# Performance work log

Measured on AMD Instinct MI355X. Metric: run time of the kernel, lower is better.

## Reference

```python
import jax, jax.numpy as jnp
import numpy as np

D_MODEL = 1024
HIDDEN = 4096
N_EXPERTS = 8
TOP_K = 2
BATCH, SEQ = 4, 4096


def setup_inputs() -> dict:
    key = jax.random.key(0)
    k1, k2, k3, k4 = jax.random.split(key, 4)
    s_in = 1.0 / np.sqrt(D_MODEL)
    s_h = 1.0 / np.sqrt(HIDDEN)
    return {
        "x": jax.random.normal(k1, (BATCH, SEQ, D_MODEL), dtype=jnp.float32),
        "gate_w": jax.random.normal(k2, (D_MODEL, N_EXPERTS), dtype=jnp.float32) * s_in,
        "w1": jax.random.normal(k3, (N_EXPERTS, D_MODEL, HIDDEN), dtype=jnp.float32) * s_in,
        "w2": jax.random.normal(k4, (N_EXPERTS, HIDDEN, D_MODEL), dtype=jnp.float32) * s_h,
    }


def reference(x, gate_w, w1, w2):
    orig_shape = x.shape
    xf = x.reshape(-1, x.shape[-1])  # [T, d]
    scores = xf @ gate_w  # [T, E]
    expert_weights, expert_indices = jax.lax.top_k(scores, TOP_K)  # [T, K]
    expert_weights = jax.nn.softmax(expert_weights, axis=-1)  # softmax over top-k only

    output = jnp.zeros_like(xf)
    for i in range(N_EXPERTS):
        # per-token combine weight for expert i (0 if not routed to i)
        sel = (expert_indices == i)  # [T, K]
        wts = jnp.sum(jnp.where(sel, expert_weights, 0.0), axis=-1)  # [T]
        h = jax.nn.silu(xf @ w1[i])  # [T, H]
        expert_out = h @ w2[i]  # [T, d]
        output = output + wts[:, None] * expert_out
    return output.reshape(orig_shape)
```

## Files before the change

kernel.cpp:

```cpp
#include <hip/hip_runtime.h>
#include <cstdint>
#include <cstddef>

#define T_TOKENS 16384
#define DMODEL 1024
#define HID 4096
#define NEXP 8
#define NPAIRS 32768

typedef _Float16 half8 __attribute__((ext_vector_type(8)));
typedef _Float16 half4 __attribute__((ext_vector_type(4)));
typedef float f32x4 __attribute__((ext_vector_type(4)));

__device__ __forceinline__ void gload_lds16(const void* g, void* l) {
  __builtin_amdgcn_global_load_lds(
      (const __attribute__((address_space(1))) unsigned int*)g,
      (__attribute__((address_space(3))) unsigned int*)l, 16, 0, 0);
}

__global__ __launch_bounds__(256) void k_gate(const float* __restrict__ x,
                                              const float* __restrict__ gw,
                                              int2* __restrict__ route_e,
                                              float2* __restrict__ route_w,
                                              int* __restrict__ counts) {
  __shared__ int lcnt[NEXP];
  int tid = threadIdx.x, lane = tid & 63, w = tid >> 6;
  if (tid < NEXP) lcnt[tid] = 0;
  __syncthreads();
  int t = blockIdx.x * 4 + w;
  const float4* xr = (const float4*)(x + (size_t)t * DMODEL);
  double s[NEXP];
#pragma unroll
  for (int e = 0; e < NEXP; e++) s[e] = 0.0;
#pragma unroll
  for (int j = 0; j < 4; j++) {
    float4 v = xr[lane + 64 * j];
    int d0 = (lane + 64 * j) * 4;
    const float* vv = (const float*)&v;
#pragma unroll
    for (int q = 0; q < 4; q++) {
      float xv = vv[q];
      const float4* g = (const float4*)(gw + (size_t)(d0 + q) * NEXP);
      float4 g0 = g[0], g1 = g[1];
      s[0] += (double)xv * g0.x; s[1] += (double)xv * g0.y;
      s[2] += (double)xv * g0.z; s[3] += (double)xv * g0.w;
      s[4] += (double)xv * g1.x; s[5] += (double)xv * g1.y;
      s[6] += (double)xv * g1.z; s[7] += (double)xv * g1.w;
    }
  }
  for (int m = 1; m < 64; m <<= 1) {
#pragma unroll
    for (int e = 0; e < NEXP; e++) s[e] += __shfl_xor(s[e], m);
  }
  if (lane == 0) {
    double m0 = -1e300; int e0 = 0;
#pragma unroll
    for (int e = 0; e < NEXP; e++) if (s[e] > m0) { m0 = s[e]; e0 = e; }
    double m1 = -1e300; int e1 = (e0 == 0) ? 1 : 0;
#pragma unroll
    for (int e = 0; e < NEXP; e++) if (e != e0 && s[e] > m1) { m1 = s[e]; e1 = e; }
    double ew = exp(m1 - m0);
    float w0 = (float)(1.0 / (1.0 + ew));
    float w1v = (float)(ew / (1.0 + ew));
    route_e[t] = make_int2(e0, e1);
    route_w[t] = make_float2(w0, w1v);
    atomicAdd(&lcnt[e0], 1);
    atomicAdd(&lcnt[e1], 1);
  }
  __syncthreads();
  if (tid < NEXP && lcnt[tid]) atomicAdd(&counts[tid], lcnt[tid]);
}

__global__ void k_prefix(const int* __restrict__ counts, int* __restrict__ offsets,
                         int* __restrict__ cursors) {
  if (threadIdx.x == 0) {
    int a = 0;
    for (int e = 0; e < NEXP; e++) { offsets[e] = a; cursors[e] = a; a += counts[e]; }
  }
}

__global__ __launch_bounds__(256) void k_assign(const int2* __restrict__ route_e,
                                                const float2* __restrict__ route_w,
                                                int* __restrict__ cursors,
                                                int* __restrict__ tok,
                                                float* __restrict__ wtp) {
  __shared__ int lcnt[NEXP];
  __shared__ int lbase[NEXP];
  int tid = threadIdx.x;
  int t = blockIdx.x * 256 + tid;
  if (tid < NEXP) lcnt[tid] = 0;
  __syncthreads();
  int2 e = route_e[t];
  float2 w = route_w[t];
  int r0 = atomicAdd(&lcnt[e.x], 1);
  int r1 = atomicAdd(&lcnt[e.y], 1);
  __syncthreads();
  if (tid < NEXP) lbase[tid] = lcnt[tid] ? atomicAdd(&cursors[tid], lcnt[tid]) : 0;
  __syncthreads();
  int p0 = lbase[e.x] + r0; tok[p0] = t; wtp[p0] = w.x;
  int p1 = lbase[e.y] + r1; tok[p1] = t; wtp[p1] = w.y;
}

__global__ __launch_bounds__(256) void k_cvt_x(const float* __restrict__ x,
                                               _Float16* __restrict__ xh) {
  int i = blockIdx.x * 256 + threadIdx.x;
  float4 v = ((const float4*)x)[i];
  half4 o = { (_Float16)v.x, (_Float16)v.y, (_Float16)v.z, (_Float16)v.w };
  ((half4*)xh)[i] = o;
}

__global__ __launch_bounds__(256) void k_tcvt(const float* __restrict__ in,
                                              _Float16* __restrict__ out,
                                              int R, int C) {
  __shared__ _Float16 tile[64][72];
  int e = blockIdx.z, tc = blockIdx.x, tr = blockIdx.y;
  const float* src = in + ((size_t)e * R + (size_t)tr * 64) * C + (size_t)tc * 64;
  int rr = threadIdx.x >> 4, c4 = (threadIdx.x & 15) * 4;
#pragma unroll
  for (int it = 0; it < 4; it++) {
    int r = rr + it * 16;
    float4 v = *(const float4*)(src + (size_t)r * C + c4);
    tile[r][c4 + 0] = (_Float16)v.x; tile[r][c4 + 1] = (_Float16)v.y;
    tile[r][c4 + 2] = (_Float16)v.z; tile[r][c4 + 3] = (_Float16)v.w;
  }
  __syncthreads();
  _Float16* dst = out + ((size_t)e * C + (size_t)tc * 64) * R + (size_t)tr * 64;
#pragma unroll
  for (int it = 0; it < 4; it++) {
    int c = rr + it * 16;
    half4 o = { tile[c4 + 0][c], tile[c4 + 1][c], tile[c4 + 2][c], tile[c4 + 3][c] };
    *(half4*)(dst + (size_t)c * R + c4) = o;
  }
}

template <int MODE>
__global__ __launch_bounds__(256) void k_gemm(
    const _Float16* __restrict__ A, const _Float16* __restrict__ B,
    const int* __restrict__ counts, const int* __restrict__ offsets,
    const int* __restrict__ tok, const float* __restrict__ wtp,
    _Float16* __restrict__ Hout, float* __restrict__ out,
    int A_stride, int B_row_stride, int B_k_off, int K_len, int n0_global, int CH) {
  int e = blockIdx.x >> 7;
  int tm = blockIdx.x & 127;
  int n_e = counts[e];
  if (tm * 128 >= n_e) return;
  int seg = offsets[e];

  __shared__ _Float16 As[128 * 64];
  __shared__ _Float16 Bs[128 * 64];

  int tid = threadIdx.x, lane = tid & 63, wid = tid >> 6;
  int wr = wid >> 1, wc = wid & 1;
  int colbase = n0_global + blockIdx.y * 128;

  const _Float16* asrc[4];
  const _Float16* bsrc[4];
  const _Float16* Bexp = B + (size_t)e * ((size_t)DMODEL * HID);
#pragma unroll
  for (int c = 0; c < 4; c++) {
    int rloc = wid * 32 + c * 8 + (lane >> 3);
    int ridx = min(tm * 128 + rloc, n_e - 1);
    size_t arow;
    if (MODE == 0) arow = (size_t)tok[seg + ridx];
    else           arow = (size_t)(seg + ridx);
    asrc[c] = A + arow * (size_t)A_stride + ((lane & 7) * 8);
    int nloc = wid * 32 + c * 8 + (lane >> 3);
    bsrc[c] = Bexp + (size_t)(colbase + nloc) * B_row_stride + B_k_off + ((lane & 7) * 8);
  }

  f32x4 acc[4][4];
#pragma unroll
  for (int m = 0; m < 4; m++)
#pragma unroll
    for (int n = 0; n < 4; n++) acc[m][n] = (f32x4){0.f, 0.f, 0.f, 0.f};

  for (int k0 = 0; k0 < K_len; k0 += 64) {
#pragma unroll
    for (int c = 0; c < 4; c++) {
      gload_lds16(asrc[c] + k0, As + (wid * 4 + c) * 512);
      gload_lds16(bsrc[c] + k0, Bs + (wid * 4 + c) * 512);
    }
    __syncthreads();
#pragma unroll
    for (int kk = 0; kk < 64; kk += 32) {
      half8 af[4], bf[4];
#pragma unroll
      for (int m = 0; m < 4; m++)
        af[m] = *(const half8*)(As + (wr * 64 + m * 16 + (lane & 15)) * 64 + kk + ((lane >> 4) * 8));
#pragma unroll
      for (int n = 0; n < 4; n++)
        bf[n] = *(const half8*)(Bs + (wc * 64 + n * 16 + (lane & 15)) * 64 + kk + ((lane >> 4) * 8));
#pragma unroll
      for (int m = 0; m < 4; m++)
#pragma unroll
        for (int n = 0; n < 4; n++)
          acc[m][n] = __builtin_amdgcn_mfma_f32_16x16x32_f16(af[m], bf[n], acc[m][n], 0, 0, 0);
    }
    __syncthreads();
  }

  int cbase = wc * 64 + (lane & 15);
#pragma unroll
  for (int m = 0; m < 4; m++) {
    int rb = wr * 64 + m * 16 + ((lane >> 4) << 2);
#pragma unroll
    for (int r = 0; r < 4; r++) {
      int grow = tm * 128 + rb + r;
      if (grow >= n_e) continue;
      int gp = seg + grow;
      if (MODE == 0) {
        _Float16* hrow = Hout + (size_t)gp * CH + blockIdx.y * 128 + cbase;
#pragma unroll
        for (int n = 0; n < 4; n++) {
          float v = acc[m][n][r];
          float sv = v / (1.f + __expf(-v));
          hrow[n * 16] = (_Float16)sv;
        }
      } else {
        float wt = wtp[gp];
        int t = tok[gp];
        float* orow = out + (size_t)t * DMODEL + colbase + cbase;
#pragma unroll
        for (int n = 0; n < 4; n++)
          atomicAdd(orow + n * 16, wt * acc[m][n][r]);
      }
    }
  }
}

extern "C" void kernel_launch(void* const* d_in, const int* in_sizes, int n_in,
                              void* d_out, int out_size, void* d_ws, size_t ws_size,
                              hipStream_t stream) {
  const float* x  = (const float*)d_in[0];
  const float* gw = (const float*)d_in[1];
  const float* w1 = (const float*)d_in[2];
  const float* w2 = (const float*)d_in[3];
  float* out = (float*)d_out;

  char* p = (char*)d_ws;
  int* counts  = (int*)p;
  int* cursors = (int*)(p + 64);
  int* offsets = (int*)(p + 128);
  p += 4096;
  int2*   route_e = (int2*)p;   p += (size_t)T_TOKENS * 8;
  float2* route_w = (float2*)p; p += (size_t)T_TOKENS * 8;
  int*    tok = (int*)p;        p += (size_t)NPAIRS * 4;
  float*  wtp = (float*)p;      p += (size_t)NPAIRS * 4;
  _Float16* xh  = (_Float16*)p; p += (size_t)T_TOKENS * DMODEL * 2;
  _Float16* w1T = (_Float16*)p; p += (size_t)NEXP * DMODEL * HID * 2;
  _Float16* w2T = (_Float16*)p; p += (size_t)NEXP * DMODEL * HID * 2;
  size_t used = (size_t)(p - (char*)d_ws);
  int CH = HID;
  while (CH > 256 && used + (size_t)NPAIRS * CH * 2 > ws_size) CH >>= 1;
  _Float16* Hbuf = (_Float16*)p;

  hipMemsetAsync(counts, 0, 4096, stream);
  hipMemsetAsync(out, 0, (size_t)out_size * 4, stream);

  k_cvt_x<<<T_TOKENS * DMODEL / 4 / 256, 256, 0, stream>>>(x, xh);
  k_tcvt<<<dim3(HID / 64, DMODEL / 64, NEXP), 256, 0, stream>>>(w1, w1T, DMODEL, HID);
  k_tcvt<<<dim3(DMODEL / 64, HID / 64, NEXP), 256, 0, stream>>>(w2, w2T, HID, DMODEL);
  k_gate<<<T_TOKENS / 4, 256, 0, stream>>>(x, gw, route_e, route_w, counts);
  k_prefix<<<1, 64, 0, stream>>>(counts, offsets, cursors);
  k_assign<<<T_TOKENS / 256, 256, 0, stream>>>(route_e, route_w, cursors, tok, wtp);

  for (int h0 = 0; h0 < HID; h0 += CH) {
    k_gemm<0><<<dim3(NEXP * 128, CH / 128), 256, 0, stream>>>(
        xh, w1T, counts, offsets, tok, wtp, Hbuf, nullptr,
        DMODEL, DMODEL, 0, DMODEL, h0, CH);
    k_gemm<1><<<dim3(NEXP * 128, DMODEL / 128), 256, 0, stream>>>(
        Hbuf, w2T, counts, offsets, tok, wtp, nullptr, out,
        CH, HID, h0, CH, 0, CH);
  }
}
```

Measured before the change: 1.591 ms.

## Enlarge grouped GEMM tiles to 256x256 with triple-buffered async LDS pipeline

Reworks the expert GEMM kernel to use 512-thread blocks computing 256x256 output tiles, with each wave holding an 8x4 grid of MFMA accumulators. The K loop now runs in 32-wide steps through a three-stage LDS ring filled by global_load_lds, prefetching two steps ahead and using explicit vmcnt waits, barriers and setprio around the MFMA block. The goals are more data reuse per LDS load and overlap of global memory traffic with compute. The costs are higher register and LDS use (96 KB of LDS per block), fewer blocks in flight, and more wasted work on partly filled 256-row expert tiles.

```diff
diff --git a/kernel.cpp b/kernel.cpp
--- a/kernel.cpp
+++ b/kernel.cpp
@@ -134,95 +134,134 @@
 }
 
 template <int MODE>
-__global__ __launch_bounds__(256) void k_gemm(
+__global__ __launch_bounds__(512, 2) void k_gemm(
     const _Float16* __restrict__ A, const _Float16* __restrict__ B,
     const int* __restrict__ counts, const int* __restrict__ offsets,
     const int* __restrict__ tok, const float* __restrict__ wtp,
     _Float16* __restrict__ Hout, float* __restrict__ out,
-    int A_stride, int B_row_stride, int B_k_off, int K_len, int n0_global, int CH) {
+    int A_stride, int B_row_stride, int B_k_off, int NT, int n0_global, int CH) {
   int e = blockIdx.x >> 7;
   int tm = blockIdx.x & 127;
   int n_e = counts[e];
-  if (tm * 128 >= n_e) return;
+  if (tm * 256 >= n_e) return;
   int seg = offsets[e];
 
-  __shared__ _Float16 As[128 * 64];
-  __shared__ _Float16 Bs[128 * 64];
+  __shared__ _Float16 lds[49152];
 
   int tid = threadIdx.x, lane = tid & 63, wid = tid >> 6;
-  int wr = wid >> 1, wc = wid & 1;
-  int colbase = n0_global + blockIdx.y * 128;
-
-  const _Float16* asrc[4];
-  const _Float16* bsrc[4];
+  int wr = wid >> 2, wc = wid & 3;
+  int ri = lane & 15, ks = lane >> 4;
+  int colbase = n0_global + blockIdx.y * 256;
   const _Float16* Bexp = B + (size_t)e * ((size_t)DMODEL * HID);
-#pragma unroll
-  for (int c = 0; c < 4; c++) {
-    int rloc = wid * 32 + c * 8 + (lane >> 3);
-    int ridx = min(tm * 128 + rloc, n_e - 1);
-    size_t arow;
-    if (MODE == 0) arow = (size_t)tok[seg + ridx];
-    else           arow = (size_t)(seg + ridx);
-    asrc[c] = A + arow * (size_t)A_stride + ((lane & 7) * 8);
-    int nloc = wid * 32 + c * 8 + (lane >> 3);
-    bsrc[c] = Bexp + (size_t)(colbase + nloc) * B_row_stride + B_k_off + ((lane & 7) * 8);
-  }
-
-  f32x4 acc[4][4];
-#pragma unroll
-  for (int m = 0; m < 4; m++)
+
+  const _Float16* aptr0;
+  const _Float16* aptr1;
+  const _Float16* bptr0;
+  const _Float16* bptr1;
+  {
+    int lr0 = (2 * wid) * 16 + ri, lr1 = (2 * wid + 1) * 16 + ri;
+    int row0 = min(tm * 256 + lr0, n_e - 1);
+    int row1 = min(tm * 256 + lr1, n_e - 1);
+    size_t ar0, ar1;
+    if (MODE == 0) { ar0 = (size_t)tok[seg + row0]; ar1 = (size_t)tok[seg + row1]; }
+    else           { ar0 = (size_t)(seg + row0);    ar1 = (size_t)(seg + row1); }
+    aptr0 = A + ar0 * (size_t)A_stride + ks * 8;
+    aptr1 = A + ar1 * (size_t)A_stride + ks * 8;
+    bptr0 = Bexp + (size_t)(colbase + lr0) * B_row_stride + B_k_off + ks * 8;
+    bptr1 = Bexp + (size_t)(colbase + lr1) * B_row_stride + B_k_off + ks * 8;
+  }
+
+#define STAGE(kt, b) do { \
+    const size_t _ko = (size_t)(kt) * 32; \
+    _Float16* _ab = lds + (b) * 16384 + (2 * wid) * 512; \
+    _Float16* _bb = lds + (b) * 16384 + 8192 + (2 * wid) * 512; \
+    gload_lds16(aptr0 + _ko, _ab); \
+    gload_lds16(aptr1 + _ko, _ab + 512); \
+    gload_lds16(bptr0 + _ko, _bb); \
+    gload_lds16(bptr1 + _ko, _bb + 512); \
+  } while (0)
+
+  f32x4 acc[8][4];
+#pragma unroll
+  for (int m = 0; m < 8; m++)
 #pragma unroll
     for (int n = 0; n < 4; n++) acc[m][n] = (f32x4){0.f, 0.f, 0.f, 0.f};
 
-  for (int k0 = 0; k0 < K_len; k0 += 64) {
-#pragma unroll
-    for (int c = 0; c < 4; c++) {
-      gload_lds16(asrc[c] + k0, As + (wid * 4 + c) * 512);
-      gload_lds16(bsrc[c] + k0, Bs + (wid * 4 + c) * 512);
+  STAGE(0, 0);
+  STAGE(1, 1);
+  asm volatile("s_waitcnt vmcnt(4)" ::: "memory");
+  __builtin_amdgcn_s_barrier();
+  __builtin_amdgcn_sched_barrier(0);
+
+  int cur = 0, nx2 = 2;
+  for (int kt = 0; kt < NT; ++kt) {
+    const _Float16* Ac = lds + cur * 16384 + (wr * 8) * 512 + lane * 8;
+    const _Float16* Bc = lds + cur * 16384 + 8192 + (wc * 4) * 512 + lane * 8;
+    half8 af[8], bf[4];
+#pragma unroll
+    for (int m = 0; m < 8; m++) af[m] = *(const half8*)(Ac + m * 512);
+#pragma unroll
+    for (int n = 0; n < 4; n++) bf[n] = *(const half8*)(Bc + n * 512);
+
+    if (kt + 2 < NT) {
+      STAGE(kt + 2, nx2);
+      __builtin_amdgcn_sched_barrier(0);
+      asm volatile("s_waitcnt vmcnt(4)" ::: "memory");
+    } else {
+      asm volatile("s_waitcnt vmcnt(0)" ::: "memory");
     }
-    __syncthreads();
-#pragma unroll
-    for (int kk = 0; kk < 64; kk += 32) {
-      half8 af[4], bf[4];
-#pragma unroll
-      for (int m = 0; m < 4; m++)
-        af[m] = *(const half8*)(As + (wr * 64 + m * 16 + (lane & 15)) * 64 + kk + ((lane >> 4) * 8));
+    __builtin_amdgcn_s_barrier();
+    __builtin_amdgcn_sched_barrier(0);
+
+    __builtin_amdgcn_s_setprio(1);
+#pragma unroll
+    for (int m = 0; m < 8; m++)
 #pragma unroll
       for (int n = 0; n < 4; n++)
-        bf[n] = *(const half8*)(Bs + (wc * 64 + n * 16 + (lane & 15)) * 64 + kk + ((lane >> 4) * 8));
-#pragma unroll
-      for (int m = 0; m < 4; m++)
-#pragma unroll
-        for (int n = 0; n < 4; n++)
-          acc[m][n] = __builtin_amdgcn_mfma_f32_16x16x32_f16(af[m], bf[n], acc[m][n], 0, 0, 0);
+        acc[m][n] = __builtin_amdgcn_mfma_f32_16x16x32_f16(af[m], bf[n], acc[m][n], 0, 0, 0);
+    __builtin_amdgcn_s_setprio(0);
+    __builtin_amdgcn_sched_barrier(0);
+    __builtin_amdgcn_s_barrier();
+    __builtin_amdgcn_sched_barrier(0);
+
+    cur = (cur == 2) ? 0 : cur + 1;
+    nx2 = (nx2 == 2) ? 0 : nx2 + 1;
+  }
+#undef STAGE
+
+  int rem = n_e - tm * 256;
+  int cloc = blockIdx.y * 256 + wc * 64 + ri;
+  int lrow0 = wr * 128 + ks * 4;
+  if (MODE == 0) {
+#pragma unroll
+    for (int m = 0; m < 8; m++) {
+#pragma unroll
+      for (int j = 0; j < 4; j++) {
+        int lr = lrow0 + m * 16 + j;
+        if (lr >= rem) continue;
+        size_t gp = (size_t)(seg + tm * 256 + lr);
+        _Float16* hrow = Hout + gp * CH + cloc;
+#pragma unroll
+        for (int n = 0; n < 4; n++) {
+          float v = acc[m][n][j];
+          hrow[n * 16] = (_Float16)(v / (1.f + __expf(-v)));
+        }
+      }
     }
-    __syncthreads();
-  }
-
-  int cbase = wc * 64 + (lane & 15);
-#pragma unroll
-  for (int m = 0; m < 4; m++) {
-    int rb = wr * 64 + m * 16 + ((lane >> 4) << 2);
-#pragma unroll
-    for (int r = 0; r < 4; r++) {
-      int grow = tm * 128 + rb + r;
-      if (grow >= n_e) continue;
-      int gp = seg + grow;
-      if (MODE == 0) {
-        _Float16* hrow = Hout + (size_t)gp * CH + blockIdx.y * 128 + cbase;
-#pragma unroll
-        for (int n = 0; n < 4; n++) {
-          float v = acc[m][n][r];
-          float sv = v / (1.f + __expf(-v));
-          hrow[n * 16] = (_Float16)sv;
-        }
-      } else {
+  } else {
+#pragma unroll
+    for (int m = 0; m < 8; m++) {
+#pragma unroll
+      for (int j = 0; j < 4; j++) {
+        int lr = lrow0 + m * 16 + j;
+        if (lr >= rem) continue;
+        int gp = seg + tm * 256 + lr;
         float wt = wtp[gp];
         int t = tok[gp];
-        float* orow = out + (size_t)t * DMODEL + colbase + cbase;
+        float* orow = out + (size_t)t * DMODEL + n0_global + blockIdx.y * 256 + wc * 64 + ri;
 #pragma unroll
         for (int n = 0; n < 4; n++)
-          atomicAdd(orow + n * 16, wt * acc[m][n][r]);
+          atomicAdd(orow + n * 16, wt * acc[m][n][j]);
       }
     }
   }
@@ -265,11 +304,11 @@
   k_assign<<<T_TOKENS / 256, 256, 0, stream>>>(route_e, route_w, cursors, tok, wtp);
 
   for (int h0 = 0; h0 < HID; h0 += CH) {
-    k_gemm<0><<<dim3(NEXP * 128, CH / 128), 256, 0, stream>>>(
+    k_gemm<0><<<dim3(NEXP * 128, CH / 256), 512, 0, stream>>>(
         xh, w1T, counts, offsets, tok, wtp, Hbuf, nullptr,
-        DMODEL, DMODEL, 0, DMODEL, h0, CH);
-    k_gemm<1><<<dim3(NEXP * 128, DMODEL / 128), 256, 0, stream>>>(
+        DMODEL, DMODEL, 0, DMODEL / 32, h0, CH);
+    k_gemm<1><<<dim3(NEXP * 128, DMODEL / 256), 512, 0, stream>>>(
         Hbuf, w2T, counts, offsets, tok, wtp, nullptr, out,
-        CH, HID, h0, CH, 0, CH);
-  }
-}
+        CH, HID, h0, CH / 32, 0, CH);
+  }
+}
```

Measured after the change: 1.902 ms. +19.5%, slower.
